# Performance work log

Measured on AMD Instinct MI355X. Metric: run time of the kernel, lower is better.

The kernel has to match this reference:

```python
import jax, jax.numpy as jnp
import numpy as np

B, L = 2, 5            # batches (scenes) and cavs per scene (fixed record_len)
THRESHOLD = 0.01       # communication threshold (eval path)
K_SIZE, SIGMA = 5, 1.0 # fixed gaussian smoothing filter


def _gaussian_kernel():
    c = K_SIZE // 2
    xx, yy = np.mgrid[0 - c:K_SIZE - c, 0 - c:K_SIZE - c]
    k = 1.0 / (2.0 * np.pi * SIGMA) * np.exp(-(np.square(xx) + np.square(yy)) / (2.0 * SIGMA ** 2))
    return jnp.asarray(k, jnp.float32)[None, None]  # OIHW (1,1,k,k)


def setup_inputs() -> dict:
    key = jax.random.key(0)
    ks = jax.random.split(key, 9)
    N, C, H, W, A = B * L, 64, 128, 256, 2
    return {
        "x": jax.random.normal(ks[0], (N, C, H, W), jnp.float32),
        "psm_single": jax.random.normal(ks[1], (N, A, H, W), jnp.float32),
        "inv_delay": jax.random.uniform(ks[2], (N,), jnp.float32, 0.1, 5.0),
        "ew_w": jax.random.normal(ks[3], (1,), jnp.float32),
        "ew_b": jax.random.normal(ks[4], (1,), jnp.float32),
        "ewc_w": jax.random.normal(ks[5], (1,), jnp.float32),
        "ewc_b": jax.random.normal(ks[6], (1,), jnp.float32),
        "sta_w1": jax.random.normal(ks[7], (4, 64), jnp.float32) * 0.1,
        "sta_w2": jax.random.normal(ks[8], (64, 4), jnp.float32) * 0.1,
    }


def reference(x, psm_single, inv_delay, ew_w, ew_b, ewc_w, ewc_b, sta_w1, sta_w2):
    N, C, H, W = x.shape
    dt = x.dtype

    # EnhanceWeight: per-cav AoI gate tanh(fc(1/(delay+0.1))) + 1
    enw = jnp.tanh(inv_delay * ew_w[0] + ew_b[0]) + 1.0          # (N,)
    x = x * enw[:, None, None, None]

    # Communication: sigmoid confidence, max over anchors, AoI gate, gaussian smooth
    conf = jax.nn.sigmoid(psm_single).max(axis=1, keepdims=True)  # (N,1,H,W)
    enc = jnp.tanh(inv_delay * ewc_w[0] + ewc_b[0]) + 1.0
    conf = conf * enc[:, None, None, None]
    conf = jax.lax.conv_general_dilated(
        conf, _gaussian_kernel().astype(dt), (1, 1), 'SAME',
        dimension_numbers=('NCHW', 'OIHW', 'NCHW'))
    mask = (conf > THRESHOLD).astype(dt)                          # (N,1,H,W)
    mask = mask.reshape(B, L, 1, H, W).at[:, 0].set(1.0)          # ego always communicates
    comm_rate = mask.mean()

    xm = x.reshape(B, L, C, H, W) * mask                          # masked per-cav features

    # TransformerFusion: per-pixel cross-agent attention, keep ego (row 0) output only
    feats = xm.transpose(0, 3, 4, 1, 2).reshape(B, H * W, L, C)   # (B, P, L, C)
    scale = 1.0 / jnp.sqrt(jnp.asarray(C, dt))
    scores = jnp.einsum('bpc,bplc->bpl', feats[:, :, 0], feats) * scale
    attn = jax.nn.softmax(scores, axis=-1)                        # (B, P, L)
    fused = jnp.einsum('bpl,bplc->bpc', attn, feats)              # (B, P, C)
    x_fuse = fused.transpose(0, 2, 1).reshape(B, C, H, W)

    # ShortTermAttention: channel gate from shared MLP over avg- and max-pooled stats
    def fc(v):  # v: (B, C)
        return jax.nn.relu(v @ sta_w1.T) @ sta_w2.T

    avg = x_fuse.mean(axis=(2, 3))
    mx = x_fuse.max(axis=(2, 3))
    gate = jax.nn.sigmoid(fc(avg) + fc(mx))                       # (B, C)
    out = x_fuse * gate[:, :, None, None]
    return out, comm_rate
```

## Files before the change

kernel.cpp:

```cpp
#include <hip/hip_runtime.h>
#include <math.h>

#define BB 2
#define LL 5
#define NN 10
#define CC 64
#define HH 128
#define WW 256
#define PP (HH*WW)
#define NP (NN*PP)


__global__ __launch_bounds__(256) void k_attnfuse(const float* __restrict__ x,
                                                  const float* __restrict__ psm,
                                                  const float* __restrict__ inv_delay,
                                                  const float* __restrict__ ew_w,
                                                  const float* __restrict__ ew_b,
                                                  const float* __restrict__ ewc_w,
                                                  const float* __restrict__ ewc_b,
                                                  float* __restrict__ out,
                                                  float* __restrict__ partS,
                                                  float* __restrict__ partM,
                                                  float* __restrict__ cntp) {
    const float g0 = 0.15915494309189535f;
    const float g1 = 0.09653235263005391f;
    const float g2 = 0.05854983152431917f;
    const float g4 = 0.02153927930184936f;
    const float g5 = 0.01306423328468446f;
    const float g8 = 0.00291502449738744f;
    const float G[25] = { g8,g5,g4,g5,g8,
                          g5,g2,g1,g2,g5,
                          g4,g1,g0,g1,g4,
                          g5,g2,g1,g2,g5,
                          g8,g5,g4,g5,g8 };

    int blk = blockIdx.x;
    int b   = blk >> 9;
    int tid  = threadIdx.x;
    int lane = tid & 63;
    int wv   = tid >> 6;
    int pblock = blk & 511;
    int p = (pblock << 6) + lane;
    int h  = pblock >> 2;
    int c0 = (pblock & 3) << 6;

    __shared__ float cs[5 * 5 * 68];
    __shared__ float encs[5], enws[5];
    if (tid < 5)
        encs[tid] = tanhf(inv_delay[b * LL + tid] * ewc_w[0] + ewc_b[0]) + 1.0f;
    else if (tid < 10)
        enws[tid - 5] = tanhf(inv_delay[b * LL + tid - 5] * ew_w[0] + ew_b[0]) + 1.0f;
    __syncthreads();

    for (int idx = tid; idx < 1700; idx += 256) {
        int l   = idx / 340;
        int rem = idx - l * 340;
        int r   = rem / 68;
        int cc2 = rem - r * 68;
        int row = h - 2 + r;
        int col = c0 - 2 + cc2;
        float v = 0.0f;
        if ((unsigned)row < (unsigned)HH && (unsigned)col < (unsigned)WW) {
            int n = b * LL + l;
            float a0 = psm[(n * 2 + 0) * PP + row * WW + col];
            float a1 = psm[(n * 2 + 1) * PP + row * WW + col];
            v = fmaxf(1.0f / (1.0f + expf(-a0)), 1.0f / (1.0f + expf(-a1))) * encs[l];
        }
        cs[idx] = v;
    }
    __syncthreads();

    float mv[5];
#pragma unroll
    for (int l = 0; l < LL; ++l) {
        float acc = 0.0f;
#pragma unroll
        for (int r = 0; r < 5; ++r)
#pragma unroll
            for (int dx = 0; dx < 5; ++dx)
                acc += cs[l * 340 + r * 68 + lane + dx] * G[r * 5 + dx];
        mv[l] = (acc > 0.01f) ? 1.0f : 0.0f;
    }
    mv[0] = 1.0f;

    if (wv == 0) {
        float v = mv[0] + mv[1] + mv[2] + mv[3] + mv[4];
#pragma unroll
        for (int o = 32; o > 0; o >>= 1) v += __shfl_down(v, o, 64);
        if (lane == 0) cntp[blk] = v;
    }

    const float* xb = x + b * (LL * CC * PP) + p;
    int cbase = wv << 4;

    float xr[16][5];
    float s5[5] = {0.f, 0.f, 0.f, 0.f, 0.f};
#pragma unroll
    for (int cc = 0; cc < 16; ++cc) {
        const float* xc = xb + (cbase + cc) * PP;
#pragma unroll
        for (int l = 0; l < LL; ++l) xr[cc][l] = xc[l * CC * PP];
        float q = xr[cc][0];
#pragma unroll
        for (int l = 0; l < LL; ++l) s5[l] += q * xr[cc][l];
    }

    __shared__ float sred[4][5][64];
#pragma unroll
    for (int l = 0; l < LL; ++l) sred[wv][l][lane] = s5[l];
    __syncthreads();

    float a[5];
    {
        float m[5], t[5], sc[5], e[5];
#pragma unroll
        for (int l = 0; l < LL; ++l) {
            t[l] = sred[0][l][lane] + sred[1][l][lane] + sred[2][l][lane] + sred[3][l][lane];
            m[l] = enws[l] * mv[l];
        }
        const float scale = 0.125f;
#pragma unroll
        for (int l = 0; l < LL; ++l) sc[l] = t[l] * m[0] * m[l] * scale;
        float mxv = fmaxf(fmaxf(fmaxf(sc[0], sc[1]), fmaxf(sc[2], sc[3])), sc[4]);
        float sum = 0.f;
#pragma unroll
        for (int l = 0; l < LL; ++l) { e[l] = expf(sc[l] - mxv); sum += e[l]; }
        float inv = 1.0f / sum;
#pragma unroll
        for (int l = 0; l < LL; ++l) a[l] = e[l] * inv * m[l];
    }

    float* ob = out + b * (CC * PP) + p;
#pragma unroll
    for (int cc = 0; cc < 16; ++cc) {
        float f = 0.f;
#pragma unroll
        for (int l = 0; l < LL; ++l) f += a[l] * xr[cc][l];
        ob[(cbase + cc) * PP] = f;

        float sv = f, mm = f;
#pragma unroll
        for (int o = 1; o < 64; o <<= 1) {
            sv += __shfl_xor(sv, o, 64);
            mm = fmaxf(mm, __shfl_xor(mm, o, 64));
        }
        if (lane == 0) {
            partS[blk * CC + cbase + cc] = sv;
            partM[blk * CC + cbase + cc] = mm;
        }
    }
}

__global__ __launch_bounds__(256) void k_finish(const float* __restrict__ partS,
                                                const float* __restrict__ partM,
                                                const float* __restrict__ cntp,
                                                const float* __restrict__ w1,
                                                const float* __restrict__ w2,
                                                float* __restrict__ gate,
                                                float* __restrict__ comm_out) {
    int t = threadIdx.x;
    int pair = t >> 1;
    int sub  = t & 1;
    __shared__ float sS[2][128], sM[2][128];
    {
        int b = pair >> 6, c = pair & 63;
        float s = 0.f, m = -INFINITY;
        int base = b * 512 + sub * 256;
        for (int pb = 0; pb < 256; ++pb) {
            int i = (base + pb) * CC + c;
            s += partS[i];
            m = fmaxf(m, partM[i]);
        }
        sS[sub][pair] = s;
        sM[sub][pair] = m;
    }
    __syncthreads();
    __shared__ float stA[128], stM[128];
    if (t < 128) {
        stA[t] = (sS[0][t] + sS[1][t]) * (1.0f / (float)PP);
        stM[t] = fmaxf(sM[0][t], sM[1][t]);
    }
    __syncthreads();
    __shared__ float hs[BB][4];
    if (t < BB * 4) {
        int b = t >> 2, j = t & 3;
        float ha = 0.f, hm = 0.f;
        for (int c = 0; c < CC; ++c) {
            float wv = w1[j * CC + c];
            ha += stA[b * CC + c] * wv;
            hm += stM[b * CC + c] * wv;
        }
        hs[b][j] = fmaxf(ha, 0.0f) + fmaxf(hm, 0.0f);
    }
    __syncthreads();
    if (t < 128) {
        int b = t >> 6, c = t & 63;
        float g = hs[b][0] * w2[c * 4 + 0] + hs[b][1] * w2[c * 4 + 1]
                + hs[b][2] * w2[c * 4 + 2] + hs[b][3] * w2[c * 4 + 3];
        gate[t] = 1.0f / (1.0f + expf(-g));
    }
    float s = 0.f;
    for (int j = t; j < 1024; j += 256) s += cntp[j];
#pragma unroll
    for (int o = 32; o > 0; o >>= 1) s += __shfl_down(s, o, 64);
    __shared__ float cred[4];
    if ((t & 63) == 0) cred[t >> 6] = s;
    __syncthreads();
    if (t == 0)
        comm_out[0] = (cred[0] + cred[1] + cred[2] + cred[3]) * (1.0f / (float)NP);
}

__global__ __launch_bounds__(256) void k_scale(float* __restrict__ out,
                                               const float* __restrict__ gate) {
    int idx = blockIdx.x * 256 + threadIdx.x;
    int bc = idx >> 13;
    float g = gate[bc];
    float4 v = ((float4*)out)[idx];
    v.x *= g; v.y *= g; v.z *= g; v.w *= g;
    ((float4*)out)[idx] = v;
}

extern "C" void kernel_launch(void* const* d_in, const int* in_sizes, int n_in,
                              void* d_out, int out_size, void* d_ws, size_t ws_size,
                              hipStream_t stream) {
    const float* x         = (const float*)d_in[0];
    const float* psm       = (const float*)d_in[1];
    const float* inv_delay = (const float*)d_in[2];
    const float* ew_w      = (const float*)d_in[3];
    const float* ew_b      = (const float*)d_in[4];
    const float* ewc_w     = (const float*)d_in[5];
    const float* ewc_b     = (const float*)d_in[6];
    const float* w1        = (const float*)d_in[7];
    const float* w2        = (const float*)d_in[8];
    float* out = (float*)d_out;
    float* wsf = (float*)d_ws;

    float* gate  = wsf;
    float* cntp  = wsf + 128;
    float* partS = wsf + 2048;
    float* partM = wsf + 2048 + 1024 * CC;

    k_attnfuse<<<1024, 256, 0, stream>>>(x, psm, inv_delay, ew_w, ew_b, ewc_w, ewc_b,
                                         out, partS, partM, cntp);
    k_finish<<<1, 256, 0, stream>>>(partS, partM, cntp, w1, w2, gate, out + BB * CC * PP);
    k_scale<<<BB * CC * PP / 4 / 256, 256, 0, stream>>>(out, gate);
}
```

Measured before the change: 56.10 us.

## Split confidence mask into separate kernel and widen attention blocks to 512 threads

Moves the sigmoid, gaussian-smoothing and threshold mask computation out of the attention kernel into its own row-per-block kernel that writes the mask to workspace. The attention kernel then reads the mask directly and uses 512-thread blocks with 8 channels per wave. The aim is to remove the redundant psm halo loads and the stencil work from the bandwidth-bound fuse kernel and to add parallelism per pixel block. In exchange it adds a kernel launch and a write and read of the mask through memory.

```diff
diff --git a/kernel.cpp b/kernel.cpp
--- a/kernel.cpp
+++ b/kernel.cpp
@@ -11,16 +11,11 @@
 #define NP (NN*PP)
 
 
-__global__ __launch_bounds__(256) void k_attnfuse(const float* __restrict__ x,
-                                                  const float* __restrict__ psm,
+__global__ __launch_bounds__(256) void k_confmask(const float* __restrict__ psm,
                                                   const float* __restrict__ inv_delay,
-                                                  const float* __restrict__ ew_w,
-                                                  const float* __restrict__ ew_b,
                                                   const float* __restrict__ ewc_w,
                                                   const float* __restrict__ ewc_b,
-                                                  float* __restrict__ out,
-                                                  float* __restrict__ partS,
-                                                  float* __restrict__ partM,
+                                                  float* __restrict__ mask,
                                                   float* __restrict__ cntp) {
     const float g0 = 0.15915494309189535f;
     const float g1 = 0.09653235263005391f;
@@ -33,70 +28,72 @@
                           g4,g1,g0,g1,g4,
                           g5,g2,g1,g2,g5,
                           g8,g5,g4,g5,g8 };
-
+    int blk = blockIdx.x;
+    int n   = blk >> 7;
+    int h   = blk & 127;
+    int t   = threadIdx.x;
+    float enc = tanhf(inv_delay[n] * ewc_w[0] + ewc_b[0]) + 1.0f;
+    const float* pn0 = psm + (n * 2 + 0) * PP;
+    const float* pn1 = psm + (n * 2 + 1) * PP;
+
+    __shared__ float cs[5][WW];
+#pragma unroll
+    for (int r = 0; r < 5; ++r) {
+        int row = h - 2 + r;
+        float v = 0.0f;
+        if ((unsigned)row < (unsigned)HH) {
+            float a0 = pn0[row * WW + t];
+            float a1 = pn1[row * WW + t];
+            v = fmaxf(1.0f / (1.0f + expf(-a0)), 1.0f / (1.0f + expf(-a1))) * enc;
+        }
+        cs[r][t] = v;
+    }
+    __syncthreads();
+
+    float acc = 0.0f;
+#pragma unroll
+    for (int r = 0; r < 5; ++r) {
+#pragma unroll
+        for (int dx = -2; dx <= 2; ++dx) {
+            int col = t + dx;
+            if ((unsigned)col < (unsigned)WW)
+                acc += cs[r][col] * G[r * 5 + (dx + 2)];
+        }
+    }
+    float mv = (acc > 0.01f) ? 1.0f : 0.0f;
+    if ((n % LL) == 0) mv = 1.0f;
+    mask[n * PP + h * WW + t] = mv;
+
+    float v = mv;
+#pragma unroll
+    for (int o = 32; o > 0; o >>= 1) v += __shfl_down(v, o, 64);
+    __shared__ float sred[4];
+    int lane = t & 63, wid = t >> 6;
+    if (lane == 0) sred[wid] = v;
+    __syncthreads();
+    if (t == 0) cntp[blk] = sred[0] + sred[1] + sred[2] + sred[3];
+}
+
+__global__ __launch_bounds__(512) void k_attnfuse(const float* __restrict__ x,
+                                                  const float* __restrict__ mask,
+                                                  const float* __restrict__ inv_delay,
+                                                  const float* __restrict__ ew_w,
+                                                  const float* __restrict__ ew_b,
+                                                  float* __restrict__ out,
+                                                  float* __restrict__ partS,
+                                                  float* __restrict__ partM) {
     int blk = blockIdx.x;
     int b   = blk >> 9;
-    int tid  = threadIdx.x;
-    int lane = tid & 63;
-    int wv   = tid >> 6;
-    int pblock = blk & 511;
-    int p = (pblock << 6) + lane;
-    int h  = pblock >> 2;
-    int c0 = (pblock & 3) << 6;
-
-    __shared__ float cs[5 * 5 * 68];
-    __shared__ float encs[5], enws[5];
-    if (tid < 5)
-        encs[tid] = tanhf(inv_delay[b * LL + tid] * ewc_w[0] + ewc_b[0]) + 1.0f;
-    else if (tid < 10)
-        enws[tid - 5] = tanhf(inv_delay[b * LL + tid - 5] * ew_w[0] + ew_b[0]) + 1.0f;
-    __syncthreads();
-
-    for (int idx = tid; idx < 1700; idx += 256) {
-        int l   = idx / 340;
-        int rem = idx - l * 340;
-        int r   = rem / 68;
-        int cc2 = rem - r * 68;
-        int row = h - 2 + r;
-        int col = c0 - 2 + cc2;
-        float v = 0.0f;
-        if ((unsigned)row < (unsigned)HH && (unsigned)col < (unsigned)WW) {
-            int n = b * LL + l;
-            float a0 = psm[(n * 2 + 0) * PP + row * WW + col];
-            float a1 = psm[(n * 2 + 1) * PP + row * WW + col];
-            v = fmaxf(1.0f / (1.0f + expf(-a0)), 1.0f / (1.0f + expf(-a1))) * encs[l];
-        }
-        cs[idx] = v;
-    }
-    __syncthreads();
-
-    float mv[5];
-#pragma unroll
-    for (int l = 0; l < LL; ++l) {
-        float acc = 0.0f;
-#pragma unroll
-        for (int r = 0; r < 5; ++r)
-#pragma unroll
-            for (int dx = 0; dx < 5; ++dx)
-                acc += cs[l * 340 + r * 68 + lane + dx] * G[r * 5 + dx];
-        mv[l] = (acc > 0.01f) ? 1.0f : 0.0f;
-    }
-    mv[0] = 1.0f;
-
-    if (wv == 0) {
-        float v = mv[0] + mv[1] + mv[2] + mv[3] + mv[4];
-#pragma unroll
-        for (int o = 32; o > 0; o >>= 1) v += __shfl_down(v, o, 64);
-        if (lane == 0) cntp[blk] = v;
-    }
-
+    int lane = threadIdx.x & 63;
+    int wv   = threadIdx.x >> 6;
+    int p = ((blk & 511) << 6) + lane;
     const float* xb = x + b * (LL * CC * PP) + p;
-    int cbase = wv << 4;
-
-    float xr[16][5];
+    int cbase = wv << 3;
+
+    float xr[8][5];
     float s5[5] = {0.f, 0.f, 0.f, 0.f, 0.f};
 #pragma unroll
-    for (int cc = 0; cc < 16; ++cc) {
+    for (int cc = 0; cc < 8; ++cc) {
         const float* xc = xb + (cbase + cc) * PP;
 #pragma unroll
         for (int l = 0; l < LL; ++l) xr[cc][l] = xc[l * CC * PP];
@@ -105,18 +102,23 @@
         for (int l = 0; l < LL; ++l) s5[l] += q * xr[cc][l];
     }
 
-    __shared__ float sred[4][5][64];
+    __shared__ float sred[8][5][64];
 #pragma unroll
     for (int l = 0; l < LL; ++l) sred[wv][l][lane] = s5[l];
     __syncthreads();
 
+    float ew0 = ew_w[0], eb0 = ew_b[0];
     float a[5];
     {
         float m[5], t[5], sc[5], e[5];
 #pragma unroll
         for (int l = 0; l < LL; ++l) {
-            t[l] = sred[0][l][lane] + sred[1][l][lane] + sred[2][l][lane] + sred[3][l][lane];
-            m[l] = enws[l] * mv[l];
+            float tl = 0.f;
+#pragma unroll
+            for (int w = 0; w < 8; ++w) tl += sred[w][l][lane];
+            t[l] = tl;
+            float en = tanhf(inv_delay[b * LL + l] * ew0 + eb0) + 1.0f;
+            m[l] = en * mask[(b * LL + l) * PP + p];
         }
         const float scale = 0.125f;
 #pragma unroll
@@ -132,7 +134,7 @@
 
     float* ob = out + b * (CC * PP) + p;
 #pragma unroll
-    for (int cc = 0; cc < 16; ++cc) {
+    for (int cc = 0; cc < 8; ++cc) {
         float f = 0.f;
 #pragma unroll
         for (int l = 0; l < LL; ++l) f += a[l] * xr[cc][l];
@@ -200,7 +202,7 @@
         gate[t] = 1.0f / (1.0f + expf(-g));
     }
     float s = 0.f;
-    for (int j = t; j < 1024; j += 256) s += cntp[j];
+    for (int j = t; j < 1280; j += 256) s += cntp[j];
 #pragma unroll
     for (int o = 32; o > 0; o >>= 1) s += __shfl_down(s, o, 64);
     __shared__ float cred[4];
@@ -239,9 +241,10 @@
     float* cntp  = wsf + 128;
     float* partS = wsf + 2048;
     float* partM = wsf + 2048 + 1024 * CC;
-
-    k_attnfuse<<<1024, 256, 0, stream>>>(x, psm, inv_delay, ew_w, ew_b, ewc_w, ewc_b,
-                                         out, partS, partM, cntp);
+    float* mask  = wsf + 139264;
+
+    k_confmask<<<NN * HH, 256, 0, stream>>>(psm, inv_delay, ewc_w, ewc_b, mask, cntp);
+    k_attnfuse<<<1024, 512, 0, stream>>>(x, mask, inv_delay, ew_w, ew_b, out, partS, partM);
     k_finish<<<1, 256, 0, stream>>>(partS, partM, cntp, w1, w2, gate, out + BB * CC * PP);
     k_scale<<<BB * CC * PP / 4 / 256, 256, 0, stream>>>(out, gate);
 }
```

Result: slower. 59.85 us (+6.7%).
